# Performance work log

Hardware: AMD Instinct MI355X
Metric: run time of the kernel (lower is better)

Reference implementation:

```python
import jax, jax.numpy as jnp
import numpy as np

EPS = 1e-15          # min-norm clamp (matches torch min_norm)
BALL_EPS = 4e-3      # float32 Poincare ball boundary eps
C = 1.0              # curvature for every layer


def _artanh(x):
    x = jnp.clip(x, -1.0 + 1e-7, 1.0 - 1e-7)
    return 0.5 * jnp.log((1.0 + x) / (1.0 - x))


def _norm(x):
    return jnp.maximum(jnp.linalg.norm(x, axis=-1, keepdims=True), EPS)


def proj(x, c):
    # clip points to stay inside the ball of radius (1-eps)/sqrt(c)
    n = _norm(x)
    maxnorm = (1.0 - BALL_EPS) / jnp.sqrt(c)
    return jnp.where(n > maxnorm, x / n * maxnorm, x)


def expmap0(u, c):
    sc = jnp.sqrt(c)
    n = _norm(u)
    return jnp.tanh(sc * n) * u / (sc * n)


def logmap0(p, c):
    sc = jnp.sqrt(c)
    n = _norm(p)
    return _artanh(sc * n) * p / (sc * n)


def mobius_add(x, y, c):
    x2 = jnp.sum(x * x, axis=-1, keepdims=True)
    y2 = jnp.sum(y * y, axis=-1, keepdims=True)
    xy = jnp.sum(x * y, axis=-1, keepdims=True)
    num = (1.0 + 2.0 * c * xy + c * y2) * x + (1.0 - c * x2) * y
    den = 1.0 + 2.0 * c * xy + (c ** 2) * x2 * y2
    return num / jnp.maximum(den, EPS)


def mobius_matvec(W, x, c):
    # torch HypLinear: mx = x @ W.T
    sc = jnp.sqrt(c)
    xn = _norm(x)
    mx = x @ W.T
    mxn = _norm(mx)
    res = jnp.tanh(mxn / xn * _artanh(sc * xn)) * mx / (mxn * sc)
    zero = jnp.all(mx == 0.0, axis=-1, keepdims=True)
    return jnp.where(zero, jnp.zeros((), dtype=res.dtype), res)


def hgc_layer(h, src, dst, w, W, b, c_in, c_out, n_nodes):
    # HypLinear
    mv = proj(mobius_matvec(W, h, c_in), c_in)
    hb = proj(expmap0(b[None, :], c_in), c_in)
    h = proj(mobius_add(mv, hb, c_in), c_in)
    # HypAgg: spmm in the tangent space at the origin
    xt = logmap0(h, c_in)                                  # [N, D]
    msg = w[:, None] * xt[src]                             # [E, D]
    agg = jax.ops.segment_sum(msg, dst, num_segments=n_nodes)
    h = proj(expmap0(agg, c_in), c_in)
    # HypAct: relu in tangent space, re-map with c_out
    xt = jax.nn.relu(logmap0(h, c_in))
    return proj(expmap0(xt, c_out), c_out)


def setup_inputs() -> dict:
    key = jax.random.key(0)
    k = jax.random.split(key, 8)
    N, E, F, D = 80000, 1280000, 256, 64
    x = jax.random.normal(k[0], (N, F), dtype=jnp.float32)
    src = jax.random.randint(k[1], (E,), 0, N)
    dst = jax.random.randint(k[2], (E,), 0, N)
    edge_weight = jax.random.uniform(k[3], (E,), dtype=jnp.float32)
    W1 = jax.random.normal(k[4], (D, F), dtype=jnp.float32) / np.sqrt(F)
    b1 = jax.random.normal(k[5], (D,), dtype=jnp.float32) * 0.01
    W2 = jax.random.normal(k[6], (D, D), dtype=jnp.float32) / np.sqrt(D)
    b2 = jax.random.normal(k[7], (D,), dtype=jnp.float32) * 0.01
    return {"x": x, "src": src, "dst": dst, "edge_weight": edge_weight,
            "W1": W1, "b1": b1, "W2": W2, "b2": b2}


def reference(x, src, dst, edge_weight, W1, b1, W2, b2):
    n_nodes = x.shape[0]
    # encode(): proj_tan0 is identity on the Poincare ball
    h = proj(expmap0(x, C), C)
    h = hgc_layer(h, src, dst, edge_weight, W1, b1, C, C, n_nodes)
    h = hgc_layer(h, src, dst, edge_weight, W2, b2, C, C, n_nodes)
    return h
```

## Files before the change

kernel.cpp:

```cpp
#include <hip/hip_runtime.h>


#define EPSV 1e-15f
#define MAXN 0.996f

typedef unsigned short bfu;
typedef __attribute__((ext_vector_type(8))) short v8s;
typedef __attribute__((ext_vector_type(4))) float v4f;

__device__ __forceinline__ bfu f2b(float f) {
    unsigned int u;
    __builtin_memcpy(&u, &f, sizeof(u));
    u += 0x7fffu + ((u >> 16) & 1u);
    return (bfu)(u >> 16);
}

__device__ __forceinline__ float b2f(bfu s) {
    unsigned int u = ((unsigned int)s) << 16;
    float f;
    __builtin_memcpy(&f, &u, sizeof(f));
    return f;
}

__device__ __forceinline__ float uplo(unsigned int u) {
// ... 45 lines not shown
    } else { mv = 0.0f; x2s = 0.0f; }
    float xy = wredsum(mv * hb);
    float ca = 1.0f + 2.0f * xy + y2;
    float cb = 1.0f - x2s;
    float den = fmaxf(1.0f + 2.0f * xy + x2s * y2, EPSV);
    float hj = (ca * mv + cb * hb) / den;
    float hn = fmaxf(sqrtf(wredsum(hj * hj)), EPSV);
    if (hn > MAXN) { hj *= MAXN / hn; hn = MAXN; }
    return (artanh_(hn) / hn) * hj;
}

__device__ __forceinline__ float agg_transform(float a, float* xn_out) {
    float n = fmaxf(sqrtf(wredsum(a * a)), EPSV);
    float th = tanhf(n);
    float g = th / n;
    float nh = fmaxf(th, EPSV);
    if (nh > MAXN) { g *= MAXN / nh; nh = MAXN; }
    float h = g * a;
    float t = fmaxf((artanh_(nh) / nh) * h, 0.0f);
    float n2 = fmaxf(sqrtf(wredsum(t * t)), EPSV);
    float th2 = tanhf(n2);
    float g2 = th2 / n2;
    float nh2 = fmaxf(th2, EPSV);
    if (nh2 > MAXN) { g2 *= MAXN / nh2; nh2 = MAXN; }
    *xn_out = nh2;
    return g2 * t;
}

__device__ __forceinline__ float bias_point(const float* bv, int lane, float* y2) {
    float b = bv[lane];
    float bn = fmaxf(sqrtf(wredsum(b * b)), EPSV);
    float gs = tanhf(bn) / bn;
    float hbn = fmaxf(tanhf(bn), EPSV);
    if (hbn > MAXN) gs *= MAXN / hbn;
    float hb = gs * b;
    *y2 = wredsum(hb * hb);
    return hb;
}

__global__ __launch_bounds__(256) void hgA_zero(float* __restrict__ p, int n4) {
    const float4 z = make_float4(0.f, 0.f, 0.f, 0.f);
    int stride = gridDim.x * blockDim.x;
    for (int i = blockIdx.x * blockDim.x + threadIdx.x; i < n4; i += stride)
        ((float4*)p)[i] = z;
}

__global__ __launch_bounds__(256) void hgA_prep(
    int* __restrict__ deg, int N,
    const float* __restrict__ W1, const float* __restrict__ W2,
    bfu* __restrict__ w1b, bfu* __restrict__ w2b, int NW1, int NW2)
{
    const int b = blockIdx.x, tid = threadIdx.x;
    if (b < 128) {
        for (int i = b * 256 + tid; i < N; i += 128 * 256) deg[i] = 0;
    } else if (b < 128 + (NW1 + 255) / 256) {
        int i = (b - 128) * 256 + tid;
        if (i < NW1) w1b[i] = f2b(W1[i]);
    } else {
        for (int i = tid; i < NW2; i += 256) w2b[i] = f2b(W2[i]);
    }
}

__device__ __forceinline__ void layer1_tail(
    int nodeBase, int m, int q, float usq, const float* hbv, float y2,
    v4f acc0, v4f acc1, v4f acc2, v4f acc3, bfu* __restrict__ xtb)
{
    float P[4], Q[4];
#pragma unroll
    for (int r = 0; r < 4; ++r) {
        float s2 = acc0[r]*acc0[r] + acc1[r]*acc1[r] + acc2[r]*acc2[r] + acc3[r]*acc3[r];
        float sh = acc0[r]*hbv[0] + acc1[r]*hbv[1] + acc2[r]*hbv[2] + acc3[r]*hbv[3];
#pragma unroll
        for (int o = 1; o < 16; o <<= 1) {
            s2 += __shfl_xor(s2, o, 64);
            sh += __shfl_xor(sh, o, 64);
        }
        float usq_r = __shfl(usq, q * 4 + r);
        float n  = fmaxf(sqrtf(usq_r), EPSV);
        float th = tanhf(n);
        float gamma = th / n;
        float xn = fmaxf(th, EPSV);
        if (xn > MAXN) { gamma *= MAXN / xn; xn = MAXN; }
        float mxn = fmaxf(gamma * sqrtf(s2), EPSV);
        float rt  = tanhf(mxn / xn * artanh_(xn));
        float k1, x2s, xy;
        if (s2 != 0.0f) {
            k1 = (rt / mxn) * gamma;
            float mvn = fmaxf(fabsf(rt), EPSV);
            if (mvn > MAXN) k1 *= MAXN / mvn;
            float cn = fminf(mvn, MAXN);
            x2s = cn * cn;
            xy  = k1 * sh;
        } else { k1 = 0.0f; x2s = 0.0f; xy = 0.0f; }
        float ca = 1.0f + 2.0f * xy + y2;
        float cb = 1.0f - x2s;
        float den = fmaxf(1.0f + 2.0f * xy + x2s * y2, EPSV);
        float hn2 = ca*ca*x2s + 2.0f*ca*cb*xy + cb*cb*y2;
        float hn = fmaxf(sqrtf(hn2) / den, EPSV);
        float hs = 1.0f;
        if (hn > MAXN) { hs = MAXN / hn; hn = MAXN; }
        float lam = artanh_(hn) / hn;
        P[r] = lam * hs * ca * k1 / den;
        Q[r] = lam * hs * cb / den;
    }
#pragma unroll
    for (int r = 0; r < 4; ++r) {
        bfu* orow = xtb + (size_t)(nodeBase + q * 4 + r) * 64 + m;
        orow[ 0] = f2b(P[r] * acc0[r] + Q[r] * hbv[0]);
        orow[16] = f2b(P[r] * acc1[r] + Q[r] * hbv[1]);
        orow[32] = f2b(P[r] * acc2[r] + Q[r] * hbv[2]);
        orow[48] = f2b(P[r] * acc3[r] + Q[r] * hbv[3]);
    }
}

__device__ __forceinline__ void layer1_body(
    int bid, int tid, const float* __restrict__ x, const bfu* __restrict__ w1b,
    const float* __restrict__ b1v, bfu* __restrict__ xtb, int N)
{
    const int lane = tid & 63, wv = tid >> 6;
    const int nodeBase = (bid * 4 + wv) * 16;
    if (nodeBase >= N) return;

    float y2;
    float hb = bias_point(b1v, lane, &y2);
    float hbv[4];
#pragma unroll
    for (int t = 0; t < 4; ++t) hbv[t] = __shfl(hb, (lane & 15) + 16 * t);

    const int m = lane & 15, q = lane >> 4;
    v4f acc0 = {0,0,0,0}, acc1 = {0,0,0,0}, acc2 = {0,0,0,0}, acc3 = {0,0,0,0};
    float usq = 0.0f;

    const float* arow = x + (size_t)(nodeBase + m) * 256 + q * 8;
    const bfu* wrow = w1b + (size_t)m * 256 + q * 8;
#pragma unroll
    for (int s = 0; s < 8; ++s) {
        float af[8];
        *(float4*)(af)     = *(const float4*)(arow + s * 32);
        *(float4*)(af + 4) = *(const float4*)(arow + s * 32 + 4);
#pragma unroll
        for (int j = 0; j < 8; ++j) usq = fmaf(af[j], af[j], usq);
        v8s a = cvt8(af);
        const bfu* wb = wrow + s * 32;
        acc0 = __builtin_amdgcn_mfma_f32_16x16x32_bf16(a, *(const v8s*)(wb), acc0, 0, 0, 0);
        acc1 = __builtin_amdgcn_mfma_f32_16x16x32_bf16(a, *(const v8s*)(wb + 16 * 256), acc1, 0, 0, 0);
        acc2 = __builtin_amdgcn_mfma_f32_16x16x32_bf16(a, *(const v8s*)(wb + 32 * 256), acc2, 0, 0, 0);
        acc3 = __builtin_amdgcn_mfma_f32_16x16x32_bf16(a, *(const v8s*)(wb + 48 * 256), acc3, 0, 0, 0);
    }
    usq += __shfl_xor(usq, 16, 64);
    usq += __shfl_xor(usq, 32, 64);
    layer1_tail(nodeBase, m, q, usq, hbv, y2, acc0, acc1, acc2, acc3, xtb);
}

__device__ __forceinline__ void layer1b_body(
    int bid, int tid, const bfu* __restrict__ xb, const float* __restrict__ usqt,
    const bfu* __restrict__ w1b, const float* __restrict__ b1v,
    bfu* __restrict__ xtb, int N)
{
    const int lane = tid & 63, wv = tid >> 6;
    const int nodeBase = (bid * 4 + wv) * 16;
    if (nodeBase >= N) return;

    float y2;
    float hb = bias_point(b1v, lane, &y2);
    float hbv[4];
#pragma unroll
    for (int t = 0; t < 4; ++t) hbv[t] = __shfl(hb, (lane & 15) + 16 * t);

    const int m = lane & 15, q = lane >> 4;
    v4f acc0 = {0,0,0,0}, acc1 = {0,0,0,0}, acc2 = {0,0,0,0}, acc3 = {0,0,0,0};
    const float usq = usqt[nodeBase + m];

    const bfu* arow = xb + (size_t)(nodeBase + m) * 256 + q * 8;
    const bfu* wrow = w1b + (size_t)m * 256 + q * 8;
#pragma unroll
    for (int s = 0; s < 8; ++s) {
        v8s a = *(const v8s*)(arow + s * 32);
        const bfu* wb = wrow + s * 32;
        acc0 = __builtin_amdgcn_mfma_f32_16x16x32_bf16(a, *(const v8s*)(wb), acc0, 0, 0, 0);
        acc1 = __builtin_amdgcn_mfma_f32_16x16x32_bf16(a, *(const v8s*)(wb + 16 * 256), acc1, 0, 0, 0);
        acc2 = __builtin_amdgcn_mfma_f32_16x16x32_bf16(a, *(const v8s*)(wb + 32 * 256), acc2, 0, 0, 0);
        acc3 = __builtin_amdgcn_mfma_f32_16x16x32_bf16(a, *(const v8s*)(wb + 48 * 256), acc3, 0, 0, 0);
    }
    layer1_tail(nodeBase, m, q, usq, hbv, y2, acc0, acc1, acc2, acc3, xtb);
}

__global__ __launch_bounds__(256) void hgA_zero_i32(int* __restrict__ p, int n) {
    int stride = gridDim.x * blockDim.x;
    for (int i = blockIdx.x * blockDim.x + threadIdx.x; i < n; i += stride) p[i] = 0;
}

__global__ __launch_bounds__(256) void hgA_count(
    const int* __restrict__ dst, int* __restrict__ deg, int E) {
    int stride = gridDim.x * blockDim.x;
    for (int e = blockIdx.x * blockDim.x + threadIdx.x; e < E; e += stride)
        atomicAdd(&deg[dst[e]], 1);
}

__global__ __launch_bounds__(256) void hgA_count_rank_l1(
    const int* __restrict__ dst, int* __restrict__ deg, int* __restrict__ rank,
    int E, int nf, int nl,
    const float* __restrict__ x, const bfu* __restrict__ w1b,
    const float* __restrict__ b1v, bfu* __restrict__ xtb, int N)
{
    const int b = blockIdx.x;
    const int mn = nf < nl ? nf : nl;
    bool isC; int idx;
    if (b < 2 * mn) { isC = !(b & 1); idx = b >> 1; }
    else            { isC = (nf > nl); idx = mn + (b - 2 * mn); }
    if (isC) {
        int e0 = (idx * 256 + threadIdx.x) * 4;
        if (e0 + 4 <= E) {
            int4 d4 = *(const int4*)(dst + e0);
            int4 r4;
            r4.x = atomicAdd(&deg[d4.x], 1);
            r4.y = atomicAdd(&deg[d4.y], 1);
            r4.z = atomicAdd(&deg[d4.z], 1);
            r4.w = atomicAdd(&deg[d4.w], 1);
            *(int4*)(rank + e0) = r4;
        } else if (e0 < E) {
            for (int e = e0; e < E; ++e) rank[e] = atomicAdd(&deg[dst[e]], 1);
        }
    } else {
        layer1_body(idx, threadIdx.x, x, w1b, b1v, xtb, N);
    }
}

__global__ __launch_bounds__(256) void hgA_count_xcvt(
    const int* __restrict__ dst, int* __restrict__ deg, int* __restrict__ rank,
    int E, int nf,
    const float* __restrict__ x, bfu* __restrict__ xb, float* __restrict__ usqt,
    int nc, int N)
{
    const int b = blockIdx.x;
    const int mn = nf < nc ? nf : nc;
    bool isC; int idx;
    if (b < 2 * mn) { isC = !(b & 1); idx = b >> 1; }
    else            { isC = (nf > nc); idx = mn + (b - 2 * mn); }
    if (isC) {
        int e0 = (idx * 256 + threadIdx.x) * 4;
        if (e0 + 4 <= E) {
            int4 d4 = *(const int4*)(dst + e0);
            int4 r4;
            r4.x = atomicAdd(&deg[d4.x], 1);
            r4.y = atomicAdd(&deg[d4.y], 1);
            r4.z = atomicAdd(&deg[d4.z], 1);
            r4.w = atomicAdd(&deg[d4.w], 1);
            *(int4*)(rank + e0) = r4;
        } else if (e0 < E) {
            for (int e = e0; e < E; ++e) rank[e] = atomicAdd(&deg[dst[e]], 1);
        }
    } else {
        const int lane = threadIdx.x & 63, wv = threadIdx.x >> 6;
        const int nodeBase = (idx * 4 + wv) * 16;
        if (nodeBase >= N) return;
        const int m = lane & 15, q = lane >> 4;
        const float* arow = x + (size_t)(nodeBase + m) * 256 + q * 8;
        bfu* orow = xb + (size_t)(nodeBase + m) * 256 + q * 8;
        float usq = 0.0f;
#pragma unroll
        for (int s = 0; s < 8; ++s) {
            float af[8];
            *(float4*)(af)     = *(const float4*)(arow + s * 32);
            *(float4*)(af + 4) = *(const float4*)(arow + s * 32 + 4);
#pragma unroll
            for (int j = 0; j < 8; ++j) usq = fmaf(af[j], af[j], usq);
            *(v8s*)(orow + s * 32) = cvt8(af);
        }
        usq += __shfl_xor(usq, 16, 64);
        usq += __shfl_xor(usq, 32, 64);
        if (lane < 16 && nodeBase + lane < N) usqt[nodeBase + lane] = usq;
    }
}

__global__ __launch_bounds__(256) void hgA_scan1(
    const int* __restrict__ deg, int* __restrict__ rowst,
    int* __restrict__ bsum, int N, int NBr,
    const bfu* __restrict__ xb, const float* __restrict__ usqt,
    const bfu* __restrict__ w1b, const float* __restrict__ b1v,
    bfu* __restrict__ xtb, int NL)
{
    if (blockIdx.x >= NBr) {
        int vb = blockIdx.x - NBr;
        if (vb < NL) layer1b_body(vb, threadIdx.x, xb, usqt, w1b, b1v, xtb, N);
        return;
    }
    __shared__ int wsum[4];
    const int tid = threadIdx.x, lane = tid & 63, wv = tid >> 6;
    const int base = blockIdx.x * 1024 + tid * 4;
    int v0 = 0, v1 = 0, v2 = 0, v3 = 0;
    if (base + 4 <= N) {
        int4 d4 = *(const int4*)(deg + base);
        v0 = d4.x; v1 = d4.y; v2 = d4.z; v3 = d4.w;
    } else {
        if (base + 0 < N) v0 = deg[base + 0];
        if (base + 1 < N) v1 = deg[base + 1];
        if (base + 2 < N) v2 = deg[base + 2];
        if (base + 3 < N) v3 = deg[base + 3];
    }
    const int tsum = v0 + v1 + v2 + v3;
    int incl = tsum;
#pragma unroll
    for (int o = 1; o < 64; o <<= 1) {
        int nb = __shfl_up(incl, o, 64);
        if (lane >= o) incl += nb;
    }
    if (lane == 63) wsum[wv] = incl;
    __syncthreads();
    int add = 0;
#pragma unroll
    for (int w = 0; w < 4; ++w) { int s = wsum[w]; if (w < wv) add += s; }
    const int excl = add + incl - tsum;
    const int e0 = excl, e1 = e0 + v0, e2 = e1 + v1, e3 = e2 + v2;
    if (base + 4 <= N) {
        *(int4*)(rowst + base) = make_int4(e0, e1, e2, e3);
    } else {
        if (base + 0 < N) rowst[base + 0] = e0;
        if (base + 1 < N) rowst[base + 1] = e1;
        if (base + 2 < N) rowst[base + 2] = e2;
        if (base + 3 < N) rowst[base + 3] = e3;
    }
    if (tid == 255) bsum[blockIdx.x] = add + incl;
}

__global__ __launch_bounds__(64) void hgA_scan2(
    int* __restrict__ bsum, int* __restrict__ tot, int NB)
{
    const int lane = threadIdx.x;
    int run = 0;
    for (int b = 0; b < NB; b += 64) {
        int i = b + lane;
        int v = (i < NB) ? bsum[i] : 0;
        int incl = v;
#pragma unroll
        for (int o = 1; o < 64; o <<= 1) {
            int nb = __shfl_up(incl, o, 64);
            if (lane >= o) incl += nb;
        }
        if (i < NB) bsum[i] = run + incl - v;
        run += __shfl(incl, 63);
    }
    if (lane == 0) *tot = run;
}

__global__ __launch_bounds__(256) void hgA_scan3(
    int* __restrict__ rowst, const int* __restrict__ bsum, int N)
{
    const int base = blockIdx.x * 1024 + threadIdx.x * 4;
    const int off = bsum[blockIdx.x];
    if (base + 4 <= N) {
        int4 r = *(int4*)(rowst + base);
        r.x += off; r.y += off; r.z += off; r.w += off;
        *(int4*)(rowst + base) = r;
    } else {
        for (int i = base; i < N; ++i) rowst[i] += off;
    }
}

__global__ __launch_bounds__(1024) void hgA_scan_l1(
    const int* __restrict__ deg, int* __restrict__ row_start,
    int* __restrict__ cursor, int N,
    const float* __restrict__ x, const bfu* __restrict__ w1b,
    const float* __restrict__ b1v, bfu* __restrict__ xtb, int NL)
{
    if (blockIdx.x != 0) {
        int vb = (blockIdx.x - 1) * 4 + (threadIdx.x >> 8);
        if (vb < NL) layer1_body(vb, threadIdx.x & 255, x, w1b, b1v, xtb, N);
        return;
    }
    __shared__ int wsum[16];
    __shared__ int srun;
    const int tid = threadIdx.x, lane = tid & 63, wv = tid >> 6;
    if (tid == 0) srun = 0;
    __syncthreads();
    for (int base = 0; base < N; base += 1024) {
        int i = base + tid;
        int v = (i < N) ? deg[i] : 0;
        int incl = v;
#pragma unroll
        for (int o = 1; o < 64; o <<= 1) {
            int nbr = __shfl_up(incl, o, 64);
            if (lane >= o) incl += nbr;
        }
        if (lane == 63) wsum[wv] = incl;
        __syncthreads();
        int add = 0;
#pragma unroll
        for (int w = 0; w < 16; ++w) { int s = wsum[w]; if (w < wv) add += s; }
        int excl = srun + add + incl - v;
        if (i < N) { row_start[i] = excl; cursor[i] = excl; }
        __syncthreads();
        if (tid == 1023) srun += add + incl;
        __syncthreads();
    }
    if (tid == 0) row_start[N] = srun;
}

__global__ __launch_bounds__(256) void hgA_fill_layer1(
    const int* __restrict__ src, const int* __restrict__ dst,
    const float* __restrict__ ew, int* __restrict__ cursor,
    int2* __restrict__ csr, int E, int fillBlocks,
    const float* __restrict__ x, const bfu* __restrict__ w1b,
    const float* __restrict__ b1v, bfu* __restrict__ xtb, int N)
{
    const int b = blockIdx.x;
    if (b < fillBlocks) {
        int stride = fillBlocks * blockDim.x;
        for (int e = b * blockDim.x + threadIdx.x; e < E; e += stride) {
            int d = dst[e];
            int slot = atomicAdd(&cursor[d], 1);
            csr[slot] = make_int2(src[e], f2i(ew[e]));
        }
    } else {
        layer1_body(b - fillBlocks, threadIdx.x, x, w1b, b1v, xtb, N);
    }
}

__global__ __launch_bounds__(256) void hgA_fillr_layer1(
    const int* __restrict__ src, const int* __restrict__ dst,
    const float* __restrict__ ew, const int* __restrict__ rank,
    const int* __restrict__ row_start, int2* __restrict__ csr,
    int E, int nf, int nl, int l1off,
    const float* __restrict__ x, const bfu* __restrict__ w1b,
    const float* __restrict__ b1v, bfu* __restrict__ xtb, int N)
{
    const int b = blockIdx.x;
    const int mn = nf < nl ? nf : nl;
    bool isFill; int idx;
    if (b < 2 * mn) { isFill = !(b & 1); idx = b >> 1; }
    else            { isFill = (nf > nl); idx = mn + (b - 2 * mn); }
    if (isFill) {
        int e0 = (idx * 256 + threadIdx.x) * 4;
        if (e0 + 4 <= E) {
            int4  d4 = *(const int4*)(dst + e0);
            int4  s4 = *(const int4*)(src + e0);
            int4  r4 = *(const int4*)(rank + e0);
            float4 w4 = *(const float4*)(ew + e0);
            csr[row_start[d4.x] + r4.x] = make_int2(s4.x, f2i(w4.x));
            csr[row_start[d4.y] + r4.y] = make_int2(s4.y, f2i(w4.y));
            csr[row_start[d4.z] + r4.z] = make_int2(s4.z, f2i(w4.z));
            csr[row_start[d4.w] + r4.w] = make_int2(s4.w, f2i(w4.w));
        } else if (e0 < E) {
            for (int e = e0; e < E; ++e)
                csr[row_start[dst[e]] + rank[e]] = make_int2(src[e], f2i(ew[e]));
        }
    } else {
        layer1_body(l1off + idx, threadIdx.x, x, w1b, b1v, xtb, N);
    }
}

__global__ __launch_bounds__(256) void hgA_fillr_l1b(
    const int* __restrict__ src, const int* __restrict__ dst,
    const float* __restrict__ ew, const int* __restrict__ rank,
    const int* __restrict__ row_start, int2* __restrict__ csr,
    int E, int nf, int nl, int l1off,
    const bfu* __restrict__ xb, const float* __restrict__ usqt,
    const bfu* __restrict__ w1b, const float* __restrict__ b1v,
    bfu* __restrict__ xtb, int N)
{
    const int b = blockIdx.x;
    const int mn = nf < nl ? nf : nl;
    bool isFill; int idx;
    if (b < 2 * mn) { isFill = !(b & 1); idx = b >> 1; }
    else            { isFill = (nf > nl); idx = mn + (b - 2 * mn); }
    if (isFill) {
        int e0 = (idx * 256 + threadIdx.x) * 4;
        if (e0 + 4 <= E) {
            int4  d4 = *(const int4*)(dst + e0);
            int4  s4 = *(const int4*)(src + e0);
            int4  r4 = *(const int4*)(rank + e0);
            float4 w4 = *(const float4*)(ew + e0);
            csr[row_start[d4.x] + r4.x] = make_int2(s4.x, f2i(w4.x));
            csr[row_start[d4.y] + r4.y] = make_int2(s4.y, f2i(w4.y));
            csr[row_start[d4.z] + r4.z] = make_int2(s4.z, f2i(w4.z));
            csr[row_start[d4.w] + r4.w] = make_int2(s4.w, f2i(w4.w));
        } else if (e0 < E) {
            for (int e = e0; e < E; ++e)
                csr[row_start[dst[e]] + rank[e]] = make_int2(src[e], f2i(ew[e]));
        }
    } else {
        layer1b_body(l1off + idx, threadIdx.x, xb, usqt, w1b, b1v, xtb, N);
    }
}

#define GACC_G16(T64, CSR, N0, N1, SL, GBASE, AX, AY, AZ, AW)                  \
    {                                                                          \
        float bx=0.f,by=0.f,bz=0.f,bw=0.f;                                     \
        for (int base = (N0); base < (N1); base += 16) {                       \
            int cnt = (N1) - base; if (cnt > 16) cnt = 16;                     \
            int sL = 0; float wL = 0.0f;                                       \
            if ((SL) < cnt) { int2 rec = (CSR)[base + (SL)];                   \
                              sL = rec.x; wL = i2f(rec.y); }                   \
            int j = 0;                                                         \
            for (; j + 8 <= cnt; j += 8) {                                     \
                int   s0 = __shfl(sL, (GBASE)+j  , 64), s1 = __shfl(sL, (GBASE)+j+1, 64); \
                int   s2 = __shfl(sL, (GBASE)+j+2, 64), s3 = __shfl(sL, (GBASE)+j+3, 64); \
                int   s4 = __shfl(sL, (GBASE)+j+4, 64), s5 = __shfl(sL, (GBASE)+j+5, 64); \
                int   s6 = __shfl(sL, (GBASE)+j+6, 64), s7 = __shfl(sL, (GBASE)+j+7, 64); \
                float w0 = __shfl(wL, (GBASE)+j  , 64), w1 = __shfl(wL, (GBASE)+j+1, 64); \
                float w2 = __shfl(wL, (GBASE)+j+2, 64), w3 = __shfl(wL, (GBASE)+j+3, 64); \
                float w4 = __shfl(wL, (GBASE)+j+4, 64), w5 = __shfl(wL, (GBASE)+j+5, 64); \
                float w6 = __shfl(wL, (GBASE)+j+6, 64), w7 = __shfl(wL, (GBASE)+j+7, 64); \
                uint2 u0 = (T64)[(size_t)s0 * 16 + (SL)];                      \
                uint2 u1 = (T64)[(size_t)s1 * 16 + (SL)];                      \
                uint2 u2 = (T64)[(size_t)s2 * 16 + (SL)];                      \
                uint2 u3 = (T64)[(size_t)s3 * 16 + (SL)];                      \
                uint2 u4 = (T64)[(size_t)s4 * 16 + (SL)];                      \
                uint2 u5 = (T64)[(size_t)s5 * 16 + (SL)];                      \
                uint2 u6 = (T64)[(size_t)s6 * 16 + (SL)];                      \
                uint2 u7 = (T64)[(size_t)s7 * 16 + (SL)];                      \
                AX = fmaf(w0, uplo(u0.x), AX); AY = fmaf(w0, uphi(u0.x), AY);  \
                AZ = fmaf(w0, uplo(u0.y), AZ); AW = fmaf(w0, uphi(u0.y), AW);  \
                bx = fmaf(w1, uplo(u1.x), bx); by = fmaf(w1, uphi(u1.x), by);  \
                bz = fmaf(w1, uplo(u1.y), bz); bw = fmaf(w1, uphi(u1.y), bw);  \
                AX = fmaf(w2, uplo(u2.x), AX); AY = fmaf(w2, uphi(u2.x), AY);  \
                AZ = fmaf(w2, uplo(u2.y), AZ); AW = fmaf(w2, uphi(u2.y), AW);  \
                bx = fmaf(w3, uplo(u3.x), bx); by = fmaf(w3, uphi(u3.x), by);  \
                bz = fmaf(w3, uplo(u3.y), bz); bw = fmaf(w3, uphi(u3.y), bw);  \
                AX = fmaf(w4, uplo(u4.x), AX); AY = fmaf(w4, uphi(u4.x), AY);  \
                AZ = fmaf(w4, uplo(u4.y), AZ); AW = fmaf(w4, uphi(u4.y), AW);  \
                bx = fmaf(w5, uplo(u5.x), bx); by = fmaf(w5, uphi(u5.x), by);  \
                bz = fmaf(w5, uplo(u5.y), bz); bw = fmaf(w5, uphi(u5.y), bw);  \
                AX = fmaf(w6, uplo(u6.x), AX); AY = fmaf(w6, uphi(u6.x), AY);  \
                AZ = fmaf(w6, uplo(u6.y), AZ); AW = fmaf(w6, uphi(u6.y), AW);  \
                bx = fmaf(w7, uplo(u7.x), bx); by = fmaf(w7, uphi(u7.x), by);  \
                bz = fmaf(w7, uplo(u7.y), bz); bw = fmaf(w7, uphi(u7.y), bw);  \
            }                                                                  \
            for (; j < cnt; j += 4) {            \
                int   s0 = __shfl(sL, (GBASE)+j  , 64), s1 = __shfl(sL, (GBASE)+j+1, 64); \
                int   s2 = __shfl(sL, (GBASE)+j+2, 64), s3 = __shfl(sL, (GBASE)+j+3, 64); \
                float w0 = __shfl(wL, (GBASE)+j  , 64), w1 = __shfl(wL, (GBASE)+j+1, 64); \
                float w2 = __shfl(wL, (GBASE)+j+2, 64), w3 = __shfl(wL, (GBASE)+j+3, 64); \
                uint2 u0 = (T64)[(size_t)s0 * 16 + (SL)];                      \
                uint2 u1 = (T64)[(size_t)s1 * 16 + (SL)];                      \
                uint2 u2 = (T64)[(size_t)s2 * 16 + (SL)];                      \
                uint2 u3 = (T64)[(size_t)s3 * 16 + (SL)];                      \
                AX = fmaf(w0, uplo(u0.x), AX); AY = fmaf(w0, uphi(u0.x), AY);  \
                AZ = fmaf(w0, uplo(u0.y), AZ); AW = fmaf(w0, uphi(u0.y), AW);  \
                bx = fmaf(w1, uplo(u1.x), bx); by = fmaf(w1, uphi(u1.x), by);  \
                bz = fmaf(w1, uplo(u1.y), bz); bw = fmaf(w1, uphi(u1.y), bw);  \
                AX = fmaf(w2, uplo(u2.x), AX); AY = fmaf(w2, uphi(u2.x), AY);  \
                AZ = fmaf(w2, uplo(u2.y), AZ); AW = fmaf(w2, uphi(u2.y), AW);  \
                bx = fmaf(w3, uplo(u3.x), bx); by = fmaf(w3, uphi(u3.x), by);  \
                bz = fmaf(w3, uplo(u3.y), bz); bw = fmaf(w3, uphi(u3.y), bw);  \
            }                                                                  \
        }                                                                      \
        AX += bx; AY += by; AZ += bz; AW += bw;                                \
    }

__global__ __launch_bounds__(256) void hgA_gather(
    const int* __restrict__ row_start, const int2* __restrict__ csr,
    const bfu* __restrict__ xtb, float* __restrict__ agg, int N) {
    const int lane = threadIdx.x & 63, wv = threadIdx.x >> 6;
    const int g = lane >> 4, sl = lane & 15, gbase = g << 4;
    const int d = (blockIdx.x * 4 + wv) * 4 + g;
    if (d >= N) return;
    const uint2* t64 = (const uint2*)xtb;
    const int n0 = row_start[d], n1 = row_start[d + 1];
    float ax = 0.f, ay = 0.f, az = 0.f, aw = 0.f;
    GACC_G16(t64, csr, n0, n1, sl, gbase, ax, ay, az, aw);
    *(float4*)(agg + (size_t)d * 64 + 4 * sl) = make_float4(ax, ay, az, aw);
}

__global__ __launch_bounds__(256) void hgA_gather_out(
    const int* __restrict__ row_start, const int2* __restrict__ csr,
    const bfu* __restrict__ xtb2, float* __restrict__ out, int N) {
    const int lane = threadIdx.x & 63, wv = threadIdx.x >> 6;
    const int g = lane >> 4, sl = lane & 15, gbase = g << 4;
    const int d = (blockIdx.x * 4 + wv) * 4 + g;
    if (d >= N) return;
    const uint2* t64 = (const uint2*)xtb2;
    const int n0 = row_start[d], n1 = row_start[d + 1];
    float t0 = 0.f, t1 = 0.f, t2 = 0.f, t3 = 0.f;
    GACC_G16(t64, csr, n0, n1, sl, gbase, t0, t1, t2, t3);
    float ssq = t0*t0 + t1*t1 + t2*t2 + t3*t3;
#pragma unroll
    for (int o = 1; o < 16; o <<= 1) ssq += __shfl_xor(ssq, o, 64);
    float n  = fmaxf(sqrtf(ssq), EPSV);
    float th = tanhf(n);
    float gg = th / n;
    float nh = fmaxf(th, EPSV);
    if (nh > MAXN) { gg *= MAXN / nh; nh = MAXN; }
    float lamg = (artanh_(nh) / nh) * gg;
    float r0 = fmaxf(lamg * t0, 0.0f);
    float r1 = fmaxf(lamg * t1, 0.0f);
    float r2 = fmaxf(lamg * t2, 0.0f);
    float r3 = fmaxf(lamg * t3, 0.0f);
    float tsq = r0*r0 + r1*r1 + r2*r2 + r3*r3;
#pragma unroll
    for (int o = 1; o < 16; o <<= 1) tsq += __shfl_xor(tsq, o, 64);
    float n2  = fmaxf(sqrtf(tsq), EPSV);
    float th2 = tanhf(n2);
    float g2  = th2 / n2;
    float nh2 = fmaxf(th2, EPSV);
    if (nh2 > MAXN) g2 *= MAXN / nh2;
    *(float4*)(out + (size_t)d * 64 + 4 * sl) =
        make_float4(g2 * r0, g2 * r1, g2 * r2, g2 * r3);
}

__global__ __launch_bounds__(256) void hgA_layer2_mfma(
    const float* __restrict__ agg,
    const bfu* __restrict__ w2b,
    const float* __restrict__ b2v,
    bfu* __restrict__ xtb2, int N)
{
    const int tid = threadIdx.x, lane = tid & 63, wv = tid >> 6;
    const int nodeBase = (blockIdx.x * 4 + wv) * 16;
    if (nodeBase >= N) return;

    float y2;
    float hb = bias_point(b2v, lane, &y2);
    float hbv[4];
#pragma unroll
    for (int t = 0; t < 4; ++t) hbv[t] = __shfl(hb, (lane & 15) + 16 * t);

    const int m = lane & 15, q = lane >> 4;
    const bool rowok = (nodeBase + m) < N;

    float af0[8], af1[8];
    const float* arow = agg + (size_t)(nodeBase + m) * 64 + q * 8;
    if (rowok) {
        *(float4*)(af0)     = *(const float4*)(arow);
        *(float4*)(af0 + 4) = *(const float4*)(arow + 4);
        *(float4*)(af1)     = *(const float4*)(arow + 32);
        *(float4*)(af1 + 4) = *(const float4*)(arow + 36);
    } else {
#pragma unroll
        for (int j = 0; j < 8; ++j) { af0[j] = 0.0f; af1[j] = 0.0f; }
    }
    float asq = 0.0f;
#pragma unroll
    for (int j = 0; j < 8; ++j) {
        asq = fmaf(af0[j], af0[j], asq);
        asq = fmaf(af1[j], af1[j], asq);
// ... 103 lines not shown
    float hbv[4];
#pragma unroll
    for (int t = 0; t < 4; ++t) hbv[t] = __shfl(hb, (lane & 15) + 16 * t);
    const int m = lane & 15, q = lane >> 4;
    v4f acc0 = {0,0,0,0}, acc1 = {0,0,0,0}, acc2 = {0,0,0,0}, acc3 = {0,0,0,0};
    float usq = 0.0f;
    const float* arow = x + (size_t)(nodeBase + m) * 256 + q * 8;
#pragma unroll
    for (int s = 0; s < 8; ++s) {
        float af[8];
        *(float4*)(af)     = *(const float4*)(arow + s * 32);
        *(float4*)(af + 4) = *(const float4*)(arow + s * 32 + 4);
#pragma unroll
        for (int j = 0; j < 8; ++j) usq = fmaf(af[j], af[j], usq);
        v8s a = cvt8(af);
        const float* wbase = W1 + (size_t)m * 256 + s * 32 + q * 8;
        float wf[8];
        *(float4*)(wf) = *(const float4*)(wbase);  *(float4*)(wf+4) = *(const float4*)(wbase+4);
        acc0 = __builtin_amdgcn_mfma_f32_16x16x32_bf16(a, cvt8(wf), acc0, 0, 0, 0);
        *(float4*)(wf) = *(const float4*)(wbase+16*256); *(float4*)(wf+4) = *(const float4*)(wbase+16*256+4);
        acc1 = __builtin_amdgcn_mfma_f32_16x16x32_bf16(a, cvt8(wf), acc1, 0, 0, 0);
        *(float4*)(wf) = *(const float4*)(wbase+32*256); *(float4*)(wf+4) = *(const float4*)(wbase+32*256+4);
        acc2 = __builtin_amdgcn_mfma_f32_16x16x32_bf16(a, cvt8(wf), acc2, 0, 0, 0);
        *(float4*)(wf) = *(const float4*)(wbase+48*256); *(float4*)(wf+4) = *(const float4*)(wbase+48*256+4);
        acc3 = __builtin_amdgcn_mfma_f32_16x16x32_bf16(a, cvt8(wf), acc3, 0, 0, 0);
    }
    usq += __shfl_xor(usq, 16, 64);
    usq += __shfl_xor(usq, 32, 64);
    float P[4], Q[4];
#pragma unroll
    for (int r = 0; r < 4; ++r) {
        float s2 = acc0[r]*acc0[r] + acc1[r]*acc1[r] + acc2[r]*acc2[r] + acc3[r]*acc3[r];
        float sh = acc0[r]*hbv[0] + acc1[r]*hbv[1] + acc2[r]*hbv[2] + acc3[r]*hbv[3];
#pragma unroll
        for (int o = 1; o < 16; o <<= 1) { s2 += __shfl_xor(s2, o, 64); sh += __shfl_xor(sh, o, 64); }
        float usq_r = __shfl(usq, q * 4 + r);
        float n  = fmaxf(sqrtf(usq_r), EPSV);
        float th = tanhf(n);
        float gamma = th / n;
        float xn = fmaxf(th, EPSV);
        if (xn > MAXN) { gamma *= MAXN / xn; xn = MAXN; }
        float mxn = fmaxf(gamma * sqrtf(s2), EPSV);
        float rt  = tanhf(mxn / xn * artanh_(xn));
        float k1, x2s, xy;
        if (s2 != 0.0f) {
            k1 = (rt / mxn) * gamma;
            float mvn = fmaxf(fabsf(rt), EPSV);
            if (mvn > MAXN) k1 *= MAXN / mvn;
            float cn = fminf(mvn, MAXN);
            x2s = cn * cn; xy = k1 * sh;
        } else { k1 = 0.0f; x2s = 0.0f; xy = 0.0f; }
        float ca = 1.0f + 2.0f * xy + y2;
        float cb = 1.0f - x2s;
        float den = fmaxf(1.0f + 2.0f * xy + x2s * y2, EPSV);
        float hn2 = ca*ca*x2s + 2.0f*ca*cb*xy + cb*cb*y2;
        float hn = fmaxf(sqrtf(hn2) / den, EPSV);
        float hs = 1.0f;
        if (hn > MAXN) { hs = MAXN / hn; hn = MAXN; }
        float lam = artanh_(hn) / hn;
        P[r] = lam * hs * ca * k1 / den;
        Q[r] = lam * hs * cb / den;
    }
#pragma unroll
    for (int r = 0; r < 4; ++r) {
        float* orow = xt + (size_t)(nodeBase + q * 4 + r) * 64 + m;
        orow[ 0] = P[r] * acc0[r] + Q[r] * hbv[0];
        orow[16] = P[r] * acc1[r] + Q[r] * hbv[1];
        orow[32] = P[r] * acc2[r] + Q[r] * hbv[2];
        orow[48] = P[r] * acc3[r] + Q[r] * hbv[3];
    }
}

__global__ __launch_bounds__(256) void hgA_scatter(
    const int* __restrict__ src, const int* __restrict__ dst,
    const float* __restrict__ ew,
    const float* __restrict__ xt, float* __restrict__ agg, int E)
{
    const int lane = threadIdx.x & 63;
    const long long wid = ((long long)blockIdx.x * blockDim.x + threadIdx.x) >> 6;
    const long long nw = ((long long)gridDim.x * blockDim.x) >> 6;
    for (long long e = wid; e < E; e += nw) {
        int s = src[e], d = dst[e];
        atomicAdd(&agg[(size_t)d * 64 + lane], ew[e] * xt[(size_t)s * 64 + lane]);
    }
}

__global__ __launch_bounds__(256) void hgA_layer2_fb(
    const float* __restrict__ agg,
    const float* __restrict__ W2, const float* __restrict__ b2v,
    float* __restrict__ xt2, int N)
{
    const int lane = threadIdx.x & 63, wv = threadIdx.x >> 6;
    float y2;
    float hb = bias_point(b2v, lane, &y2);
    const int nw = gridDim.x * 4;
    for (int i = blockIdx.x * 4 + wv; i < N; i += nw) {
        float a = agg[(size_t)i * 64 + lane];
        float xn;
        float x2 = agg_transform(a, &xn);
        float acc = 0.0f;
        const float* Wrow = W2 + (size_t)lane * 64;
        for (int s = 0; s < 64; ++s)
            acc = fmaf(__shfl(x2, s), Wrow[s], acc);
        float o = mobius_tail(acc, xn, hb, y2);
        xt2[(size_t)i * 64 + lane] = o;
    }
}

__global__ __launch_bounds__(256) void hgA_final_fb(
    const float* __restrict__ agg, float* __restrict__ out, int N)
{
    const int lane = threadIdx.x & 63, wv = threadIdx.x >> 6;
    const int nw = gridDim.x * 4;
    for (int i = blockIdx.x * 4 + wv; i < N; i += nw) {
        float a = agg[(size_t)i * 64 + lane];
        float xn;
        float o = agg_transform(a, &xn);
        out[(size_t)i * 64 + lane] = o;
    }
}

extern "C" void kernel_launch(void* const* d_in, const int* in_sizes, int n_in,
                              void* d_out, int out_size, void* d_ws, size_t ws_size,
                              hipStream_t stream)
{
    const float* x  = (const float*)d_in[0];
    const int* src  = (const int*)d_in[1];
    const int* dst  = (const int*)d_in[2];
    const float* ew = (const float*)d_in[3];
    const float* W1 = (const float*)d_in[4];
    const float* b1 = (const float*)d_in[5];
    const float* W2 = (const float*)d_in[6];
    const float* b2 = (const float*)d_in[7];

    const int Dd = in_sizes[5];
    const int Ff = in_sizes[4] / Dd;
    const int N  = in_sizes[0] / Ff;
    const int E  = in_sizes[1];
    const int NW1 = Dd * Ff;
    const int NW2 = Dd * Dd;

    float* out = (float*)d_out;
    float* agg = (float*)d_out;

    const int NB = (N + 1023) / 1024;

    const int blkT = (N + 63) / 64;
    const int blkG16 = (N + 15) / 16;
    const int blkE4 = (E + 1023) / 1024;
    const int prepG = 128 + (NW1 + 255) / 256 + 1;
    const int n4 = (N * Dd) / 4;

    size_t xtb_b = (size_t)N * Dd * 2;
    size_t xb_b  = (size_t)N * Ff * 2;
    bfu*  xtb   = (bfu*)d_ws;
    bfu*  xbA   = (bfu*)((char*)d_ws + xtb_b);
    float* usqt = (float*)((char*)d_ws + xtb_b + xb_b);
    size_t off1 = xtb_b + xb_b + (size_t)N * 4;
    int*  degA1   = (int*)((char*)d_ws + off1);
    int*  rowstA1 = degA1 + N;
    int*  rankA1  = rowstA1 + (N + 1);
    int*  bsumA1  = rankA1 + E;
    size_t w1_offA1 = (off1 + ((size_t)(2 * N + 1) + (size_t)E + (size_t)NB) * 4 + 15) & ~(size_t)15;
    bfu* w1bA1 = (bfu*)((char*)d_ws + w1_offA1);
    bfu* w2bA1 = w1bA1 + NW1;
    size_t csr_offA1 = (w1_offA1 + (size_t)(NW1 + NW2) * 2 + 7) & ~(size_t)7;
    const size_t needA1 = csr_offA1 + (size_t)E * 8;

    int*  deg    = (int*)((char*)d_ws + xtb_b);
    int*  rowst  = deg + N;
    int*  cursor = rowst + (N + 1);
    int*  rank   = cursor + N;
    int*  bsum   = rank + E;
    size_t wA_off = (xtb_b + ((size_t)(3 * N + 1) + (size_t)E + (size_t)NB) * 4 + 15) & ~(size_t)15;
    bfu* w1bA = (bfu*)((char*)d_ws + wA_off);
    bfu* w2bA = w1bA + NW1;
    size_t csr_offA = (wA_off + (size_t)(NW1 + NW2) * 2 + 7) & ~(size_t)7;
    const size_t needA2 = csr_offA + (size_t)E * 8;

    size_t wB_off = (xtb_b + (size_t)(3 * N + 1) * 4 + 15) & ~(size_t)15;
    bfu* w1bB = (bfu*)((char*)d_ws + wB_off);
    bfu* w2bB = w1bB + NW1;
    size_t csr_offB = (wB_off + (size_t)(NW1 + NW2) * 2 + 7) & ~(size_t)7;
    const size_t needB = csr_offB + (size_t)E * 8;

    if (ws_size >= needA1) {
        int2* csr = (int2*)((char*)d_ws + csr_offA1);
        int L1S = blkT < 192 ? blkT : 192;
        int L1F = blkT - L1S;
        hgA_prep      <<<prepG, 256, 0, stream>>>(degA1, N, W1, W2, w1bA1, w2bA1, NW1, NW2);
        hgA_count_xcvt<<<blkE4 + blkT, 256, 0, stream>>>(
            dst, degA1, rankA1, E, blkE4, x, xbA, usqt, blkT, N);
        hgA_scan1     <<<NB + L1S, 256, 0, stream>>>(
            degA1, rowstA1, bsumA1, N, NB, xbA, usqt, w1bA1, b1, xtb, L1S);
        hgA_scan2     <<<1, 64, 0, stream>>>(bsumA1, rowstA1 + N, NB);
        hgA_scan3     <<<NB, 256, 0, stream>>>(rowstA1, bsumA1, N);
        hgA_fillr_l1b <<<blkE4 + L1F, 256, 0, stream>>>(
            src, dst, ew, rankA1, rowstA1, csr, E, blkE4, L1F, L1S,
            xbA, usqt, w1bA1, b1, xtb, N);
        hgA_gather     <<<blkG16, 256, 0, stream>>>(rowstA1, csr, xtb, agg, N);
        hgA_layer2_mfma<<<blkT, 256, 0, stream>>>(agg, w2bA1, b2, xtb, N);
        hgA_gather_out <<<blkG16, 256, 0, stream>>>(rowstA1, csr, xtb, out, N);
    } else if (ws_size >= needA2) {
        int2* csr = (int2*)((char*)d_ws + csr_offA);
        int L1C = blkT < 780 ? blkT : 780;
        int L1F = blkT - L1C;
        hgA_prep        <<<prepG, 256, 0, stream>>>(deg, N, W1, W2, w1bA, w2bA, NW1, NW2);
        hgA_count_rank_l1<<<blkE4 + L1C, 256, 0, stream>>>(
            dst, deg, rank, E, blkE4, L1C, x, w1bA, b1, xtb, N);
        hgA_scan1       <<<NB, 256, 0, stream>>>(deg, rowst, bsum, N, NB,
                                                 (const bfu*)xtb, (const float*)deg,
                                                 w1bA, b1, xtb, 0);
        hgA_scan2       <<<1,   64, 0, stream>>>(bsum, rowst + N, NB);
        hgA_scan3       <<<NB, 256, 0, stream>>>(rowst, bsum, N);
        hgA_fillr_layer1<<<blkE4 + L1F, 256, 0, stream>>>(
            src, dst, ew, rank, rowst, csr, E, blkE4, L1F, L1C,
            x, w1bA, b1, xtb, N);
        hgA_gather     <<<blkG16, 256, 0, stream>>>(rowst, csr, xtb, agg, N);
        hgA_layer2_mfma<<<blkT, 256, 0, stream>>>(agg, w2bA, b2, xtb, N);
        hgA_gather_out <<<blkG16, 256, 0, stream>>>(rowst, csr, xtb, out, N);
    } else if (ws_size >= needB) {
        int2* csr = (int2*)((char*)d_ws + csr_offB);
        const int fillBlocks = 2048;
        hgA_prep       <<<prepG, 256, 0, stream>>>(deg, N, W1, W2, w1bB, w2bB, NW1, NW2);
        hgA_count      <<<2048, 256, 0, stream>>>(dst, deg, E);
        hgA_scan_l1    <<<1,   1024, 0, stream>>>(
            deg, rowst, cursor, N, x, w1bB, b1, xtb, 0);
        hgA_fill_layer1<<<fillBlocks + blkT, 256, 0, stream>>>(
            src, dst, ew, cursor, csr, E, fillBlocks, x, w1bB, b1, xtb, N);
        hgA_gather     <<<blkG16, 256, 0, stream>>>(rowst, csr, xtb, agg, N);
        hgA_layer2_mfma<<<blkT, 256, 0, stream>>>(agg, w2bB, b2, xtb, N);
        hgA_gather_out <<<blkG16, 256, 0, stream>>>(rowst, csr, xtb, out, N);
    } else {
        float* xt_fb  = (float*)d_out;
        float* agg_fb = (float*)d_ws;
        hgA_layer1_fp32<<<blkT, 256, 0, stream>>>(x, W1, b1, xt_fb, N);
        hgA_zero     <<<1024,  256, 0, stream>>>(agg_fb, n4);
        hgA_scatter  <<<16384, 256, 0, stream>>>(src, dst, ew, xt_fb, agg_fb, E);
        hgA_layer2_fb<<<2048,  256, 0, stream>>>(agg_fb, W2, b2, xt_fb, N);
        hgA_zero     <<<1024,  256, 0, stream>>>(agg_fb, n4);
        hgA_scatter  <<<16384, 256, 0, stream>>>(src, dst, ew, xt_fb, agg_fb, E);
        hgA_final_fb <<<2048,  256, 0, stream>>>(agg_fb, out, N);
    }
}
```

Baseline: 315.2 us.

## Drop bf16 x pre-conversion path and split layer-1 blocks across three launches

Removes the path that first converts x to bf16 in a separate pass, along with its workspace and kernels. Layer-1 projection blocks now read fp32 x directly and are spread across the count, scan1 and fill launches so that they overlap the CSR-building work. This avoids writing and rereading an N×256 bf16 copy. In exchange, each layer-1 block reads fp32 input, which is twice the bytes, and the split ratios become fixed tuning constants.

After: 316.7 us. About the same (+0.5%).

```diff
diff --git a/kernel.cpp b/kernel.cpp
--- a/kernel.cpp
+++ b/kernel.cpp
@@ -221,39 +221,6 @@
     layer1_tail(nodeBase, m, q, usq, hbv, y2, acc0, acc1, acc2, acc3, xtb);
 }
 
-__device__ __forceinline__ void layer1b_body(
-    int bid, int tid, const bfu* __restrict__ xb, const float* __restrict__ usqt,
-    const bfu* __restrict__ w1b, const float* __restrict__ b1v,
-    bfu* __restrict__ xtb, int N)
-{
-    const int lane = tid & 63, wv = tid >> 6;
-    const int nodeBase = (bid * 4 + wv) * 16;
-    if (nodeBase >= N) return;
-
-    float y2;
-    float hb = bias_point(b1v, lane, &y2);
-    float hbv[4];
-#pragma unroll
-    for (int t = 0; t < 4; ++t) hbv[t] = __shfl(hb, (lane & 15) + 16 * t);
-
-    const int m = lane & 15, q = lane >> 4;
-    v4f acc0 = {0,0,0,0}, acc1 = {0,0,0,0}, acc2 = {0,0,0,0}, acc3 = {0,0,0,0};
-    const float usq = usqt[nodeBase + m];
-
-    const bfu* arow = xb + (size_t)(nodeBase + m) * 256 + q * 8;
-    const bfu* wrow = w1b + (size_t)m * 256 + q * 8;
-#pragma unroll
-    for (int s = 0; s < 8; ++s) {
-        v8s a = *(const v8s*)(arow + s * 32);
-        const bfu* wb = wrow + s * 32;
-        acc0 = __builtin_amdgcn_mfma_f32_16x16x32_bf16(a, *(const v8s*)(wb), acc0, 0, 0, 0);
-        acc1 = __builtin_amdgcn_mfma_f32_16x16x32_bf16(a, *(const v8s*)(wb + 16 * 256), acc1, 0, 0, 0);
-        acc2 = __builtin_amdgcn_mfma_f32_16x16x32_bf16(a, *(const v8s*)(wb + 32 * 256), acc2, 0, 0, 0);
-        acc3 = __builtin_amdgcn_mfma_f32_16x16x32_bf16(a, *(const v8s*)(wb + 48 * 256), acc3, 0, 0, 0);
-    }
-    layer1_tail(nodeBase, m, q, usq, hbv, y2, acc0, acc1, acc2, acc3, xtb);
-}
-
 __global__ __launch_bounds__(256) void hgA_zero_i32(int* __restrict__ p, int n) {
     int stride = gridDim.x * blockDim.x;
     for (int i = blockIdx.x * blockDim.x + threadIdx.x; i < n; i += stride) p[i] = 0;
@@ -295,63 +262,15 @@
     }
 }
 
-__global__ __launch_bounds__(256) void hgA_count_xcvt(
-    const int* __restrict__ dst, int* __restrict__ deg, int* __restrict__ rank,
-    int E, int nf,
-    const float* __restrict__ x, bfu* __restrict__ xb, float* __restrict__ usqt,
-    int nc, int N)
-{
-    const int b = blockIdx.x;
-    const int mn = nf < nc ? nf : nc;
-    bool isC; int idx;
-    if (b < 2 * mn) { isC = !(b & 1); idx = b >> 1; }
-    else            { isC = (nf > nc); idx = mn + (b - 2 * mn); }
-    if (isC) {
-        int e0 = (idx * 256 + threadIdx.x) * 4;
-        if (e0 + 4 <= E) {
-            int4 d4 = *(const int4*)(dst + e0);
-            int4 r4;
-            r4.x = atomicAdd(&deg[d4.x], 1);
-            r4.y = atomicAdd(&deg[d4.y], 1);
-            r4.z = atomicAdd(&deg[d4.z], 1);
-            r4.w = atomicAdd(&deg[d4.w], 1);
-            *(int4*)(rank + e0) = r4;
-        } else if (e0 < E) {
-            for (int e = e0; e < E; ++e) rank[e] = atomicAdd(&deg[dst[e]], 1);
-        }
-    } else {
-        const int lane = threadIdx.x & 63, wv = threadIdx.x >> 6;
-        const int nodeBase = (idx * 4 + wv) * 16;
-        if (nodeBase >= N) return;
-        const int m = lane & 15, q = lane >> 4;
-        const float* arow = x + (size_t)(nodeBase + m) * 256 + q * 8;
-        bfu* orow = xb + (size_t)(nodeBase + m) * 256 + q * 8;
-        float usq = 0.0f;
-#pragma unroll
-        for (int s = 0; s < 8; ++s) {
-            float af[8];
-            *(float4*)(af)     = *(const float4*)(arow + s * 32);
-            *(float4*)(af + 4) = *(const float4*)(arow + s * 32 + 4);
-#pragma unroll
-            for (int j = 0; j < 8; ++j) usq = fmaf(af[j], af[j], usq);
-            *(v8s*)(orow + s * 32) = cvt8(af);
-        }
-        usq += __shfl_xor(usq, 16, 64);
-        usq += __shfl_xor(usq, 32, 64);
-        if (lane < 16 && nodeBase + lane < N) usqt[nodeBase + lane] = usq;
-    }
-}
-
 __global__ __launch_bounds__(256) void hgA_scan1(
     const int* __restrict__ deg, int* __restrict__ rowst,
     int* __restrict__ bsum, int N, int NBr,
-    const bfu* __restrict__ xb, const float* __restrict__ usqt,
-    const bfu* __restrict__ w1b, const float* __restrict__ b1v,
-    bfu* __restrict__ xtb, int NL)
+    const float* __restrict__ x, const bfu* __restrict__ w1b,
+    const float* __restrict__ b1v, bfu* __restrict__ xtb, int NL, int l1off)
 {
     if (blockIdx.x >= NBr) {
         int vb = blockIdx.x - NBr;
-        if (vb < NL) layer1b_body(vb, threadIdx.x, xb, usqt, w1b, b1v, xtb, N);
+        if (vb < NL) layer1_body(l1off + vb, threadIdx.x, x, w1b, b1v, xtb, N);
         return;
     }
     __shared__ int wsum[4];
@@ -515,40 +434,6 @@
         }
     } else {
         layer1_body(l1off + idx, threadIdx.x, x, w1b, b1v, xtb, N);
-    }
-}
-
-__global__ __launch_bounds__(256) void hgA_fillr_l1b(
-    const int* __restrict__ src, const int* __restrict__ dst,
-    const float* __restrict__ ew, const int* __restrict__ rank,
-    const int* __restrict__ row_start, int2* __restrict__ csr,
-    int E, int nf, int nl, int l1off,
-    const bfu* __restrict__ xb, const float* __restrict__ usqt,
-    const bfu* __restrict__ w1b, const float* __restrict__ b1v,
-    bfu* __restrict__ xtb, int N)
-{
-    const int b = blockIdx.x;
-    const int mn = nf < nl ? nf : nl;
-    bool isFill; int idx;
-    if (b < 2 * mn) { isFill = !(b & 1); idx = b >> 1; }
-    else            { isFill = (nf > nl); idx = mn + (b - 2 * mn); }
-    if (isFill) {
-        int e0 = (idx * 256 + threadIdx.x) * 4;
-        if (e0 + 4 <= E) {
-            int4  d4 = *(const int4*)(dst + e0);
-            int4  s4 = *(const int4*)(src + e0);
-            int4  r4 = *(const int4*)(rank + e0);
-            float4 w4 = *(const float4*)(ew + e0);
-            csr[row_start[d4.x] + r4.x] = make_int2(s4.x, f2i(w4.x));
-            csr[row_start[d4.y] + r4.y] = make_int2(s4.y, f2i(w4.y));
-            csr[row_start[d4.z] + r4.z] = make_int2(s4.z, f2i(w4.z));
-            csr[row_start[d4.w] + r4.w] = make_int2(s4.w, f2i(w4.w));
-        } else if (e0 < E) {
-            for (int e = e0; e < E; ++e)
-                csr[row_start[dst[e]] + rank[e]] = make_int2(src[e], f2i(ew[e]));
-        }
-    } else {
-        layer1b_body(l1off + idx, threadIdx.x, xb, usqt, w1b, b1v, xtb, N);
     }
 }
 
@@ -958,21 +843,7 @@
     const int n4 = (N * Dd) / 4;
 
     size_t xtb_b = (size_t)N * Dd * 2;
-    size_t xb_b  = (size_t)N * Ff * 2;
-    bfu*  xtb   = (bfu*)d_ws;
-    bfu*  xbA   = (bfu*)((char*)d_ws + xtb_b);
-    float* usqt = (float*)((char*)d_ws + xtb_b + xb_b);
-    size_t off1 = xtb_b + xb_b + (size_t)N * 4;
-    int*  degA1   = (int*)((char*)d_ws + off1);
-    int*  rowstA1 = degA1 + N;
-    int*  rankA1  = rowstA1 + (N + 1);
-    int*  bsumA1  = rankA1 + E;
-    size_t w1_offA1 = (off1 + ((size_t)(2 * N + 1) + (size_t)E + (size_t)NB) * 4 + 15) & ~(size_t)15;
-    bfu* w1bA1 = (bfu*)((char*)d_ws + w1_offA1);
-    bfu* w2bA1 = w1bA1 + NW1;
-    size_t csr_offA1 = (w1_offA1 + (size_t)(NW1 + NW2) * 2 + 7) & ~(size_t)7;
-    const size_t needA1 = csr_offA1 + (size_t)E * 8;
-
+    bfu*  xtb    = (bfu*)d_ws;
     int*  deg    = (int*)((char*)d_ws + xtb_b);
     int*  rowst  = deg + N;
     int*  cursor = rowst + (N + 1);
@@ -982,7 +853,7 @@
     bfu* w1bA = (bfu*)((char*)d_ws + wA_off);
     bfu* w2bA = w1bA + NW1;
     size_t csr_offA = (wA_off + (size_t)(NW1 + NW2) * 2 + 7) & ~(size_t)7;
-    const size_t needA2 = csr_offA + (size_t)E * 8;
+    const size_t needA = csr_offA + (size_t)E * 8;
 
     size_t wB_off = (xtb_b + (size_t)(3 * N + 1) * 4 + 15) & ~(size_t)15;
     bfu* w1bB = (bfu*)((char*)d_ws + wB_off);
@@ -990,37 +861,20 @@
     size_t csr_offB = (wB_off + (size_t)(NW1 + NW2) * 2 + 7) & ~(size_t)7;
     const size_t needB = csr_offB + (size_t)E * 8;
 
-    if (ws_size >= needA1) {
-        int2* csr = (int2*)((char*)d_ws + csr_offA1);
-        int L1S = blkT < 192 ? blkT : 192;
-        int L1F = blkT - L1S;
-        hgA_prep      <<<prepG, 256, 0, stream>>>(degA1, N, W1, W2, w1bA1, w2bA1, NW1, NW2);
-        hgA_count_xcvt<<<blkE4 + blkT, 256, 0, stream>>>(
-            dst, degA1, rankA1, E, blkE4, x, xbA, usqt, blkT, N);
-        hgA_scan1     <<<NB + L1S, 256, 0, stream>>>(
-            degA1, rowstA1, bsumA1, N, NB, xbA, usqt, w1bA1, b1, xtb, L1S);
-        hgA_scan2     <<<1, 64, 0, stream>>>(bsumA1, rowstA1 + N, NB);
-        hgA_scan3     <<<NB, 256, 0, stream>>>(rowstA1, bsumA1, N);
-        hgA_fillr_l1b <<<blkE4 + L1F, 256, 0, stream>>>(
-            src, dst, ew, rankA1, rowstA1, csr, E, blkE4, L1F, L1S,
-            xbA, usqt, w1bA1, b1, xtb, N);
-        hgA_gather     <<<blkG16, 256, 0, stream>>>(rowstA1, csr, xtb, agg, N);
-        hgA_layer2_mfma<<<blkT, 256, 0, stream>>>(agg, w2bA1, b2, xtb, N);
-        hgA_gather_out <<<blkG16, 256, 0, stream>>>(rowstA1, csr, xtb, out, N);
-    } else if (ws_size >= needA2) {
+    if (ws_size >= needA) {
         int2* csr = (int2*)((char*)d_ws + csr_offA);
-        int L1C = blkT < 780 ? blkT : 780;
-        int L1F = blkT - L1C;
+        int L1C = blkT < 850 ? blkT : 850;
+        int L1S = (blkT - L1C) < 250 ? (blkT - L1C) : 250;
+        int L1F = blkT - L1C - L1S;
         hgA_prep        <<<prepG, 256, 0, stream>>>(deg, N, W1, W2, w1bA, w2bA, NW1, NW2);
         hgA_count_rank_l1<<<blkE4 + L1C, 256, 0, stream>>>(
             dst, deg, rank, E, blkE4, L1C, x, w1bA, b1, xtb, N);
-        hgA_scan1       <<<NB, 256, 0, stream>>>(deg, rowst, bsum, N, NB,
-                                                 (const bfu*)xtb, (const float*)deg,
-                                                 w1bA, b1, xtb, 0);
+        hgA_scan1       <<<NB + L1S, 256, 0, stream>>>(
+            deg, rowst, bsum, N, NB, x, w1bA, b1, xtb, L1S, L1C);
         hgA_scan2       <<<1,   64, 0, stream>>>(bsum, rowst + N, NB);
         hgA_scan3       <<<NB, 256, 0, stream>>>(rowst, bsum, N);
         hgA_fillr_layer1<<<blkE4 + L1F, 256, 0, stream>>>(
-            src, dst, ew, rank, rowst, csr, E, blkE4, L1F, L1C,
+            src, dst, ew, rank, rowst, csr, E, blkE4, L1F, L1C + L1S,
             x, w1bA, b1, xtb, N);
         hgA_gather     <<<blkG16, 256, 0, stream>>>(rowst, csr, xtb, agg, N);
         hgA_layer2_mfma<<<blkT, 256, 0, stream>>>(agg, w2bA, b2, xtb, N);
```
